# Kernel tuning notes

Hardware: AMD Instinct MI355X
Metric: run time of the kernel (lower is better)

## Reference

```python
import jax, jax.numpy as jnp
import numpy as np
import math

D_MODEL = 1024
NUM_HEADS = 16
D_K = D_MODEL // NUM_HEADS
THETA = 10000.0
CONTEXT_LENGTH = 2048


def _rope_tables(seq_len):
    # freqs: [d_k/2]
    powers = jnp.arange(0, D_K, 2, dtype=jnp.float32) / D_K
    freqs = 1.0 / (THETA ** powers)
    t = jnp.arange(seq_len, dtype=jnp.float32)
    fm = jnp.outer(t, freqs)  # [s, d_k/2]
    return jnp.cos(fm), jnp.sin(fm)


def _apply_rope(x, cos, sin):
    # x: [b, h, s, d_k]; cos/sin: [s, d_k/2] broadcast to [1,1,s,d_k/2]
    c = cos[None, None, :, :].astype(x.dtype)
    s_ = sin[None, None, :, :].astype(x.dtype)
    xe = x[..., 0::2]
    xo = x[..., 1::2]
    oe = xe * c - xo * s_
    oo = xe * s_ + xo * c
    # interleave even/odd back
    out = jnp.stack([oe, oo], axis=-1).reshape(x.shape)
    return out


def setup_inputs() -> dict:
    key = jax.random.key(0)
    ks = jax.random.split(key, 5)
    b, s = 4, 2048
    std = (2.0 / (D_MODEL + D_MODEL)) ** 0.5
    x = jax.random.normal(ks[0], (b, s, D_MODEL), dtype=jnp.float32)
    Wq = jax.random.normal(ks[1], (D_MODEL, D_MODEL), dtype=jnp.float32) * std
    Wk = jax.random.normal(ks[2], (D_MODEL, D_MODEL), dtype=jnp.float32) * std
    Wv = jax.random.normal(ks[3], (D_MODEL, D_MODEL), dtype=jnp.float32) * std
    Wo = jax.random.normal(ks[4], (D_MODEL, D_MODEL), dtype=jnp.float32) * std
    return {"x": x, "Wq": Wq, "Wk": Wk, "Wv": Wv, "Wo": Wo}


def reference(x, Wq, Wk, Wv, Wo):
    b, s, d = x.shape
    h, dk = NUM_HEADS, D_K
    # projections: Linear applies x @ W.T via einsum('...i,oi->...o')
    def proj(W):
        y = jnp.einsum('bsi,oi->bso', x, W)
        return y.reshape(b, s, h, dk).transpose(0, 2, 1, 3)  # [b,h,s,dk]
    q, k, v = proj(Wq), proj(Wk), proj(Wv)
    cos, sin = _rope_tables(s)
    q = _apply_rope(q, cos, sin)
    k = _apply_rope(k, cos, sin)
    scores = jnp.einsum('bhnd,bhmd->bhnm', q, k) / math.sqrt(dk)
    causal = jnp.tril(jnp.ones((s, s), dtype=bool))
    scores = jnp.where(causal, scores, -jnp.inf)
    probs = jax.nn.softmax(scores, axis=-1)
    attn = jnp.einsum('bhnm,bhmd->bhnd', probs, v)
    attn = attn.transpose(0, 2, 1, 3).reshape(b, s, d)  # [b,s,d_model]
    return jnp.einsum('bsi,oi->bso', attn, Wo)
```

## Files before the change

kernel.cpp:

```cpp
#include <hip/hip_runtime.h>
#include <hip/hip_bf16.h>
#include <math.h>

typedef __attribute__((ext_vector_type(4))) float f32x4;
typedef __attribute__((ext_vector_type(16))) float f32x16;
typedef __attribute__((ext_vector_type(8))) short s16x8;
typedef __attribute__((ext_vector_type(4))) unsigned u32x4;

#define LDSP(p) ((__attribute__((address_space(3))) void*)(p))
#define GLBP(p) ((const __attribute__((address_space(1))) void*)(p))

__device__ __forceinline__ unsigned short f2b(float f) {
  unsigned u = __builtin_bit_cast(unsigned, f);
  u += 0x7FFFu + ((u >> 16) & 1u);
  return (unsigned short)(u >> 16);
}
__device__ __forceinline__ float b2f(unsigned short h) {
  unsigned u = ((unsigned)h) << 16;
  return __builtin_bit_cast(float, u);
}
__device__ __forceinline__ unsigned cvtpk_bf16(float lo, float hi) {
  unsigned r;
  asm("v_cvt_pk_bf16_f32 %0, %1, %2" : "=v"(r) : "v"(lo), "v"(hi));
  return r;
}

__global__ void cvt_f2b_kernel(const float* __restrict__ src, unsigned short* __restrict__ dst, int n8) {
  int i = blockIdx.x * blockDim.x + threadIdx.x;
  if (i >= n8) return;
  const float4* s = (const float4*)src;
  float4 a = s[2 * i], b = s[2 * i + 1];
  s16x8 o;
  o[0] = (short)f2b(a.x); o[1] = (short)f2b(a.y); o[2] = (short)f2b(a.z); o[3] = (short)f2b(a.w);
  o[4] = (short)f2b(b.x); o[5] = (short)f2b(b.y); o[6] = (short)f2b(b.z); o[7] = (short)f2b(b.w);
  ((s16x8*)dst)[i] = o;
}

__global__ void rope_table_kernel(float* __restrict__ cosT, float* __restrict__ sinT) {
  int idx = blockIdx.x * 256 + threadIdx.x;
  int s = idx >> 5, j = idx & 31;
  float freq = (float)(1.0 / pow(10000.0, (double)(2 * j) / 64.0));
  float fm = (float)s * freq;
  cosT[idx] = cosf(fm);
  sinT[idx] = sinf(fm);
}

__global__ void rope_apply_kernel(unsigned short* __restrict__ qk, const float* __restrict__ cosT,
                                  const float* __restrict__ sinT, float scale) {
  int i = blockIdx.x * 256 + threadIdx.x;
  int e = i * 8;
  int s = (e >> 6) & 2047;
  int jb = (e & 63) >> 1;
  s16x8 v = ((const s16x8*)qk)[i];
  float4 c = *(const float4*)(cosT + s * 32 + jb);
  float4 sn = *(const float4*)(sinT + s * 32 + jb);
  float cc[4] = {c.x, c.y, c.z, c.w}, ss[4] = {sn.x, sn.y, sn.z, sn.w};
  s16x8 o;
#pragma unroll
  for (int p = 0; p < 4; ++p) {
    float e_ = b2f((unsigned short)v[2 * p]);
    float o_ = b2f((unsigned short)v[2 * p + 1]);
    o[2 * p]     = (short)f2b((e_ * cc[p] - o_ * ss[p]) * scale);
    o[2 * p + 1] = (short)f2b((e_ * ss[p] + o_ * cc[p]) * scale);
  }
  ((s16x8*)qk)[i] = o;
}

template <int EPI>
__global__ void gemm_bt_kernel(const unsigned short* __restrict__ A, const unsigned short* __restrict__ B,
                               float* __restrict__ Cf, unsigned short* __restrict__ Cq,
                               unsigned short* __restrict__ Ck, unsigned short* __restrict__ Cv,
                               int M, int N, int K) {
  __shared__ __align__(16) unsigned short As[128 * 64];
  __shared__ __align__(16) unsigned short Bs[128 * 64];
  const int t = threadIdx.x;
  const int lane = t & 63, wave = t >> 6;
  const int wm = wave >> 1, wn = wave & 1;
  const int g = lane >> 4, q = lane & 15;
  const int m0 = blockIdx.x * 128, n0 = blockIdx.y * 128;
  const int srow = t >> 3;
  const int scol = (t & 7) << 4;
  f32x4 acc[4][4] = {};
  const int nkt = K >> 6;
  for (int kt = 0; kt < nkt; ++kt) {
    __syncthreads();
#pragma unroll
    for (int it = 0; it < 4; ++it) {
      int row = it * 32 + srow;
      int cg = scol ^ ((row & 7) << 4);
      const char* ga = (const char*)A + ((size_t)(m0 + row) * K + (kt << 6)) * 2 + cg;
      __builtin_amdgcn_global_load_lds(GLBP(ga), LDSP((char*)As + it * 4096 + wave * 1024), 16, 0, 0);
      const char* gb = (const char*)B + ((size_t)(n0 + row) * K + (kt << 6)) * 2 + cg;
      __builtin_amdgcn_global_load_lds(GLBP(gb), LDSP((char*)Bs + it * 4096 + wave * 1024), 16, 0, 0);
    }
    asm volatile("s_waitcnt vmcnt(0)" ::: "memory");
    __syncthreads();
#pragma unroll
    for (int kk = 0; kk < 2; ++kk) {
      const int colB = ((kk << 6) + (g << 4)) ^ ((q & 7) << 4);
      s16x8 af[4], bf[4];
#pragma unroll
      for (int x = 0; x < 4; ++x) {
        af[x] = *(const s16x8*)(As + (wm * 64 + x * 16 + q) * 64 + (colB >> 1));
        bf[x] = *(const s16x8*)(Bs + (wn * 64 + x * 16 + q) * 64 + (colB >> 1));
      }
#pragma unroll
      for (int mi = 0; mi < 4; ++mi)
#pragma unroll
        for (int ni = 0; ni < 4; ++ni)
          acc[mi][ni] = __builtin_amdgcn_mfma_f32_16x16x32_bf16(af[mi], bf[ni], acc[mi][ni], 0, 0, 0);
    }
  }
  if (EPI == 0) {
#pragma unroll
    for (int mi = 0; mi < 4; ++mi)
#pragma unroll
      for (int r = 0; r < 4; ++r) {
        int m = m0 + wm * 64 + mi * 16 + g * 4 + r;
#pragma unroll
        for (int ni = 0; ni < 4; ++ni) {
          int n = n0 + wn * 64 + ni * 16 + q;
          Cf[(size_t)m * N + n] = acc[mi][ni][r];
        }
      }
  } else {
    unsigned short* dst = (n0 < 1024) ? Cq : (n0 < 2048 ? Ck : Cv);
    const int obase = n0 & 1023;
#pragma unroll
    for (int mi = 0; mi < 4; ++mi)
#pragma unroll
      for (int r = 0; r < 4; ++r) {
        int m = m0 + wm * 64 + mi * 16 + g * 4 + r;
        int bb = m >> 11, s = m & 2047;
#pragma unroll
        for (int ni = 0; ni < 4; ++ni) {
          int o = obase + wn * 64 + ni * 16 + q;
          int hh = o >> 6, d = o & 63;
          dst[(((size_t)bb * 16 + hh) * 2048 + s) * 64 + d] = f2b(acc[mi][ni][r]);
        }
      }
  }
}

#define BUILD_PA(dst, SS, B) {                                        \
    unsigned X  = cvtpk_bf16(SS[B + 0], SS[B + 1]);                   \
    unsigned X2 = cvtpk_bf16(SS[B + 2], SS[B + 3]);                   \
    unsigned Y  = cvtpk_bf16(SS[B + 4], SS[B + 5]);                   \
    unsigned Y2 = cvtpk_bf16(SS[B + 6], SS[B + 7]);                   \
    asm volatile("v_permlane32_swap_b32 %0, %1" : "+v"(X), "+v"(Y));  \
    asm volatile("v_permlane32_swap_b32 %0, %1" : "+v"(X2), "+v"(Y2));\
    u32x4 pw_; pw_[0] = X; pw_[1] = X2; pw_[2] = Y; pw_[3] = Y2;      \
    dst = __builtin_bit_cast(s16x8, pw_); }

__global__ void attn_kernel(const unsigned short* __restrict__ Q, const unsigned short* __restrict__ K,
                            const unsigned short* __restrict__ V, unsigned short* __restrict__ O) {
  __shared__ __align__(16) unsigned short Ks[64 * 64];
  __shared__ __align__(16) unsigned short Vt[64 * 72];
  const int t = threadIdx.x;
  const int lane = t & 63, w = t >> 6;
  const int h = lane >> 5, ql = lane & 31;
  const int bh = blockIdx.x;
  const int qt = 15 - (int)blockIdx.y;
  const size_t hoff = (size_t)bh * 2048 * 64;
  const int q_global = qt * 128 + w * 32 + ql;
  const int qmax_w = qt * 128 + w * 32 + 31;

  s16x8 qf[4];
  {
    const unsigned short* qp = Q + hoff + (size_t)q_global * 64 + h * 8;
#pragma unroll
    for (int s = 0; s < 4; ++s) qf[s] = *(const s16x8*)(qp + 16 * s);
  }
  f32x16 accO[2] = {};
  float mrun = -3e38f, lrun = 0.f;

  const int srow = t >> 3, scol = (t & 7) << 4;
  const int ntk = 2 * qt + 2;
  for (int tk = 0; tk < ntk; ++tk) {
    __syncthreads();
    const char* kbp = (const char*)(K + hoff) + (size_t)tk * 8192;
#pragma unroll
    for (int it = 0; it < 2; ++it) {
      int row = it * 32 + srow;
      int cg = scol ^ ((row & 7) << 4);
      __builtin_amdgcn_global_load_lds(GLBP(kbp + row * 128 + cg),
                                       LDSP((char*)Ks + it * 4096 + w * 1024), 16, 0, 0);
    }
    {
      const unsigned short* vbp = V + hoff + (size_t)tk * 4096;
#pragma unroll
      for (int p = 0; p < 2; ++p) {
        int d0 = w * 8 + p * 32;
        s16x8 vv = *(const s16x8*)(vbp + lane * 64 + d0);
#pragma unroll
        for (int j = 0; j < 8; ++j) Vt[(d0 + j) * 72 + lane] = (unsigned short)vv[j];
      }
    }
    asm volatile("s_waitcnt vmcnt(0)" ::: "memory");
    __syncthreads();
    if (tk * 64 > qmax_w) continue;

    f32x16 S0 = {}, S1 = {};
#pragma unroll
    for (int s = 0; s < 4; ++s) {
      const int cb = 16 * h + 32 * s;
      const int sw = (ql & 7) << 4;
      s16x8 kf0 = *(const s16x8*)((const char*)Ks + ql * 128 + (cb ^ sw));
      S0 = __builtin_amdgcn_mfma_f32_32x32x16_bf16(kf0, qf[s], S0, 0, 0, 0);
      s16x8 kf1 = *(const s16x8*)((const char*)Ks + (32 + ql) * 128 + (cb ^ sw));
      S1 = __builtin_amdgcn_mfma_f32_32x32x16_bf16(kf1, qf[s], S1, 0, 0, 0);
    }
    if (tk * 64 + 63 > qt * 128 + w * 32) {
      const int kvb = tk * 64 + 4 * h;
#pragma unroll
      for (int r = 0; r < 16; ++r) {
        const int kvl = (r & 3) + 8 * (r >> 2);
        if (kvb + kvl > q_global) S0[r] = -3e38f;
        if (kvb + 32 + kvl > q_global) S1[r] = -3e38f;
      }
    }
    float pm = -3e38f;
#pragma unroll
    for (int r = 0; r < 16; ++r) pm = fmaxf(pm, fmaxf(S0[r], S1[r]));
    pm = fmaxf(pm, __shfl_xor(pm, 32));
    const float mnew = fmaxf(mrun, pm);
    const float alpha = exp2f(mrun - mnew);
    float ladd = 0.f;
#pragma unroll
    for (int r = 0; r < 16; ++r) {
      float p0 = exp2f(S0[r] - mnew);
      float p1 = exp2f(S1[r] - mnew);
      S0[r] = p0; S1[r] = p1;
      ladd += p0 + p1;
    }
    ladd += __shfl_xor(ladd, 32);
    lrun = lrun * alpha + ladd;
    mrun = mnew;
    if (__any(alpha < 1.0f)) {
#pragma unroll
      for (int r = 0; r < 16; ++r) {
        float ar = __shfl(alpha, 4 * h + (r & 3) + 8 * (r >> 2));
        accO[0][r] *= ar;
        accO[1][r] *= ar;
      }
    }
    s16x8 pa[4];
    BUILD_PA(pa[0], S0, 0);
    BUILD_PA(pa[1], S0, 8);
    BUILD_PA(pa[2], S1, 0);
    BUILD_PA(pa[3], S1, 8);
#pragma unroll
    for (int s = 0; s < 4; ++s) {
#pragma unroll
      for (int dt = 0; dt < 2; ++dt) {
        s16x8 vf = *(const s16x8*)(Vt + (dt * 32 + ql) * 72 + 8 * h + 16 * s);
        accO[dt] = __builtin_amdgcn_mfma_f32_32x32x16_bf16(pa[s], vf, accO[dt], 0, 0, 0);
      }
    }
  }
  const float linv = 1.0f / lrun;
  const int bb = bh >> 4, hh = bh & 15;
#pragma unroll
  for (int r = 0; r < 16; ++r) {
    const int qrow = 4 * h + (r & 3) + 8 * (r >> 2);
    const float lr = __shfl(linv, qrow);
    const int sg = qt * 128 + w * 32 + qrow;
    const size_t base = ((size_t)(bb * 2048 + sg)) * 1024 + hh * 64 + ql;
    O[base] = f2b(accO[0][r] * lr);
    O[base + 32] = f2b(accO[1][r] * lr);
  }
}

extern "C" void kernel_launch(void* const* d_in, const int* in_sizes, int n_in,
                              void* d_out, int out_size, void* d_ws, size_t ws_size,
                              hipStream_t stream) {
  const float* x  = (const float*)d_in[0];
  const float* Wq = (const float*)d_in[1];
  const float* Wk = (const float*)d_in[2];
  const float* Wv = (const float*)d_in[3];
  const float* Wo = (const float*)d_in[4];
  char* ws = (char*)d_ws;
  unsigned short* xb   = (unsigned short*)(ws);
  unsigned short* wqkv = (unsigned short*)(ws + 16777216);
  unsigned short* wo   = (unsigned short*)(ws + 23068672);
  unsigned short* qb   = (unsigned short*)(ws + 25165824);
  unsigned short* kb   = (unsigned short*)(ws + 41943040);
  unsigned short* vb   = (unsigned short*)(ws + 58720256);
  unsigned short* ab   = (unsigned short*)(ws + 75497472);
  float* cosT = (float*)(ws + 92274688);
  float* sinT = (float*)(ws + 92536832);

  cvt_f2b_kernel<<<4096, 256, 0, stream>>>(x, xb, 1048576);
  cvt_f2b_kernel<<<512, 256, 0, stream>>>(Wq, wqkv, 131072);
  cvt_f2b_kernel<<<512, 256, 0, stream>>>(Wk, wqkv + 1048576, 131072);
  cvt_f2b_kernel<<<512, 256, 0, stream>>>(Wv, wqkv + 2097152, 131072);
  cvt_f2b_kernel<<<512, 256, 0, stream>>>(Wo, wo, 131072);
  rope_table_kernel<<<256, 256, 0, stream>>>(cosT, sinT);
  gemm_bt_kernel<1><<<dim3(64, 24), 256, 0, stream>>>(xb, wqkv, nullptr, qb, kb, vb, 8192, 3072, 1024);
  rope_apply_kernel<<<4096, 256, 0, stream>>>(qb, cosT, sinT, 0.125f * 1.44269504f);
  rope_apply_kernel<<<4096, 256, 0, stream>>>(kb, cosT, sinT, 1.0f);
  attn_kernel<<<dim3(64, 16), 256, 0, stream>>>(qb, kb, vb, ab);
  gemm_bt_kernel<0><<<dim3(64, 8), 256, 0, stream>>>(ab, wo, (float*)d_out, nullptr, nullptr, nullptr, 8192, 1024, 1024);
}
```

Baseline: 277.9 us.

## Double-buffer K/V tiles in attention and add lazy softmax rescaling

```diff
diff --git a/kernel.cpp b/kernel.cpp
--- a/kernel.cpp
+++ b/kernel.cpp
@@ -154,8 +154,8 @@
 
 __global__ void attn_kernel(const unsigned short* __restrict__ Q, const unsigned short* __restrict__ K,
                             const unsigned short* __restrict__ V, unsigned short* __restrict__ O) {
-  __shared__ __align__(16) unsigned short Ks[64 * 64];
-  __shared__ __align__(16) unsigned short Vt[64 * 72];
+  __shared__ __align__(16) unsigned short Ks[2][64 * 64];
+  __shared__ __align__(16) unsigned short Vt[2][64 * 72];
   const int t = threadIdx.x;
   const int lane = t & 63, w = t >> 6;
   const int h = lane >> 5, ql = lane & 31;
@@ -175,88 +175,101 @@
   float mrun = -3e38f, lrun = 0.f;
 
   const int srow = t >> 3, scol = (t & 7) << 4;
+  const int kv0 = 2 * (lane & 31);
+  const int dbase = w * 16 + (lane >> 5) * 8;
   const int ntk = 2 * qt + 2;
-  for (int tk = 0; tk < ntk; ++tk) {
+  s16x8 va = {}, vb2 = {};
+
+  for (int it = 0; it <= ntk; ++it) {
+    const int buf = it & 1;
+    if (it < ntk) {
+      const char* kbp = (const char*)(K + hoff) + (size_t)it * 8192;
+#pragma unroll
+      for (int p = 0; p < 2; ++p) {
+        int row = p * 32 + srow;
+        int cg = scol ^ ((row & 7) << 4);
+        __builtin_amdgcn_global_load_lds(GLBP(kbp + row * 128 + cg),
+                                         LDSP((char*)Ks[buf] + p * 4096 + w * 1024), 16, 0, 0);
+      }
+      const unsigned short* vbp = V + hoff + (size_t)it * 4096;
+      va  = *(const s16x8*)(vbp + kv0 * 64 + dbase);
+      vb2 = *(const s16x8*)(vbp + (kv0 + 1) * 64 + dbase);
+    }
+    const int tkc = it - 1;
+    if (tkc >= 0 && tkc * 64 <= qmax_w) {
+      const int cb2 = tkc & 1;
+      f32x16 S0 = {}, S1 = {};
+      __builtin_amdgcn_s_setprio(1);
+#pragma unroll
+      for (int s = 0; s < 4; ++s) {
+        const int cb = 16 * h + 32 * s;
+        const int sw = (ql & 7) << 4;
+        s16x8 kf0 = *(const s16x8*)((const char*)Ks[cb2] + ql * 128 + (cb ^ sw));
+        S0 = __builtin_amdgcn_mfma_f32_32x32x16_bf16(kf0, qf[s], S0, 0, 0, 0);
+        s16x8 kf1 = *(const s16x8*)((const char*)Ks[cb2] + (32 + ql) * 128 + (cb ^ sw));
+        S1 = __builtin_amdgcn_mfma_f32_32x32x16_bf16(kf1, qf[s], S1, 0, 0, 0);
+      }
+      __builtin_amdgcn_s_setprio(0);
+      if (tkc * 64 + 63 > qt * 128 + w * 32) {
+        const int kvb = tkc * 64 + 4 * h;
+#pragma unroll
+        for (int r = 0; r < 16; ++r) {
+          const int kvl = (r & 3) + 8 * (r >> 2);
+          if (kvb + kvl > q_global) S0[r] = -3e38f;
+          if (kvb + 32 + kvl > q_global) S1[r] = -3e38f;
+        }
+      }
+      float pm = -3e38f;
+#pragma unroll
+      for (int r = 0; r < 16; ++r) pm = fmaxf(pm, fmaxf(S0[r], S1[r]));
+      pm = fmaxf(pm, __shfl_xor(pm, 32));
+      if (!__all(pm - mrun <= 8.0f)) {
+        const float mnew = fmaxf(mrun, pm);
+        const float alpha = exp2f(mrun - mnew);
+        lrun *= alpha;
+#pragma unroll
+        for (int r = 0; r < 16; ++r) {
+          float ar = __shfl(alpha, 4 * h + (r & 3) + 8 * (r >> 2));
+          accO[0][r] *= ar;
+          accO[1][r] *= ar;
+        }
+        mrun = mnew;
+      }
+      float ladd = 0.f;
+#pragma unroll
+      for (int r = 0; r < 16; ++r) {
+        float p0 = exp2f(S0[r] - mrun);
+        float p1 = exp2f(S1[r] - mrun);
+        S0[r] = p0; S1[r] = p1;
+        ladd += p0 + p1;
+      }
+      ladd += __shfl_xor(ladd, 32);
+      lrun += ladd;
+      s16x8 pa[4];
+      BUILD_PA(pa[0], S0, 0);
+      BUILD_PA(pa[1], S0, 8);
+      BUILD_PA(pa[2], S1, 0);
+      BUILD_PA(pa[3], S1, 8);
+      __builtin_amdgcn_s_setprio(1);
+#pragma unroll
+      for (int s = 0; s < 4; ++s) {
+#pragma unroll
+        for (int dt = 0; dt < 2; ++dt) {
+          s16x8 vf = *(const s16x8*)(Vt[cb2] + (dt * 32 + ql) * 72 + 8 * h + 16 * s);
+          accO[dt] = __builtin_amdgcn_mfma_f32_32x32x16_bf16(pa[s], vf, accO[dt], 0, 0, 0);
+        }
+      }
+      __builtin_amdgcn_s_setprio(0);
+    }
+    asm volatile("s_waitcnt vmcnt(0)" ::: "memory");
+    if (it < ntk) {
+#pragma unroll
+      for (int j = 0; j < 8; ++j) {
+        unsigned pk = (unsigned)(unsigned short)va[j] | ((unsigned)(unsigned short)vb2[j] << 16);
+        *(unsigned*)((char*)Vt[buf] + (size_t)((dbase + j) * 72 + kv0) * 2) = pk;
+      }
+    }
     __syncthreads();
-    const char* kbp = (const char*)(K + hoff) + (size_t)tk * 8192;
-#pragma unroll
-    for (int it = 0; it < 2; ++it) {
-      int row = it * 32 + srow;
-      int cg = scol ^ ((row & 7) << 4);
-      __builtin_amdgcn_global_load_lds(GLBP(kbp + row * 128 + cg),
-                                       LDSP((char*)Ks + it * 4096 + w * 1024), 16, 0, 0);
-    }
-    {
-      const unsigned short* vbp = V + hoff + (size_t)tk * 4096;
-#pragma unroll
-      for (int p = 0; p < 2; ++p) {
-        int d0 = w * 8 + p * 32;
-        s16x8 vv = *(const s16x8*)(vbp + lane * 64 + d0);
-#pragma unroll
-        for (int j = 0; j < 8; ++j) Vt[(d0 + j) * 72 + lane] = (unsigned short)vv[j];
-      }
-    }
-    asm volatile("s_waitcnt vmcnt(0)" ::: "memory");
-    __syncthreads();
-    if (tk * 64 > qmax_w) continue;
-
-    f32x16 S0 = {}, S1 = {};
-#pragma unroll
-    for (int s = 0; s < 4; ++s) {
-      const int cb = 16 * h + 32 * s;
-      const int sw = (ql & 7) << 4;
-      s16x8 kf0 = *(const s16x8*)((const char*)Ks + ql * 128 + (cb ^ sw));
-      S0 = __builtin_amdgcn_mfma_f32_32x32x16_bf16(kf0, qf[s], S0, 0, 0, 0);
-      s16x8 kf1 = *(const s16x8*)((const char*)Ks + (32 + ql) * 128 + (cb ^ sw));
-      S1 = __builtin_amdgcn_mfma_f32_32x32x16_bf16(kf1, qf[s], S1, 0, 0, 0);
-    }
-    if (tk * 64 + 63 > qt * 128 + w * 32) {
-      const int kvb = tk * 64 + 4 * h;
-#pragma unroll
-      for (int r = 0; r < 16; ++r) {
-        const int kvl = (r & 3) + 8 * (r >> 2);
-        if (kvb + kvl > q_global) S0[r] = -3e38f;
-        if (kvb + 32 + kvl > q_global) S1[r] = -3e38f;
-      }
-    }
-    float pm = -3e38f;
-#pragma unroll
-    for (int r = 0; r < 16; ++r) pm = fmaxf(pm, fmaxf(S0[r], S1[r]));
-    pm = fmaxf(pm, __shfl_xor(pm, 32));
-    const float mnew = fmaxf(mrun, pm);
-    const float alpha = exp2f(mrun - mnew);
-    float ladd = 0.f;
-#pragma unroll
-    for (int r = 0; r < 16; ++r) {
-      float p0 = exp2f(S0[r] - mnew);
-      float p1 = exp2f(S1[r] - mnew);
-      S0[r] = p0; S1[r] = p1;
-      ladd += p0 + p1;
-    }
-    ladd += __shfl_xor(ladd, 32);
-    lrun = lrun * alpha + ladd;
-    mrun = mnew;
-    if (__any(alpha < 1.0f)) {
-#pragma unroll
-      for (int r = 0; r < 16; ++r) {
-        float ar = __shfl(alpha, 4 * h + (r & 3) + 8 * (r >> 2));
-        accO[0][r] *= ar;
-        accO[1][r] *= ar;
-      }
-    }
-    s16x8 pa[4];
-    BUILD_PA(pa[0], S0, 0);
-    BUILD_PA(pa[1], S0, 8);
-    BUILD_PA(pa[2], S1, 0);
-    BUILD_PA(pa[3], S1, 8);
-#pragma unroll
-    for (int s = 0; s < 4; ++s) {
-#pragma unroll
-      for (int dt = 0; dt < 2; ++dt) {
-        s16x8 vf = *(const s16x8*)(Vt + (dt * 32 + ql) * 72 + 8 * h + 16 * s);
-        accO[dt] = __builtin_amdgcn_mfma_f32_32x32x16_bf16(pa[s], vf, accO[dt], 0, 0, 0);
-      }
-    }
   }
   const float linv = 1.0f / lrun;
   const int bb = bh >> 4, hh = bh & 15;
```

After: 272.7 us. Within noise of the previous version (-1.9%).
